# Kernel tuning notes

Measured on AMD Instinct MI355X. Metric: run time of the kernel, lower is better.

Reference implementation:

```python
import jax, jax.numpy as jnp
import numpy as np
import math

D_COV = 3      # covs = ['pi','juros','ipca']
WIDTH = 64     # largura default of RedeDrift/RedeDiff
T = 1024       # n_janela
I0 = 1
N_MC = 32768


def _linear_init(key, fan_in, fan_out):
    # torch nn.Linear default: U(-1/sqrt(fan_in), 1/sqrt(fan_in))
    bound = 1.0 / np.sqrt(fan_in)
    kw, kb = jax.random.split(key)
    W = jax.random.uniform(kw, (fan_in, fan_out), jnp.float32, -bound, bound)
    b = jax.random.uniform(kb, (fan_out,), jnp.float32, -bound, bound)
    return W, b


def setup_inputs() -> dict:
    key = jax.random.key(0)
    ks = jax.random.split(key, 12)
    d_in = 1 + D_COV + 1
    dW1, db1 = _linear_init(ks[0], d_in, WIDTH)
    dW2, db2 = _linear_init(ks[1], WIDTH, WIDTH)
    dW3, db3 = _linear_init(ks[2], WIDTH, 1)
    gW1, gb1 = _linear_init(ks[3], d_in, WIDTH)
    gW2, gb2 = _linear_init(ks[4], WIDTH, WIDTH)
    gW3, gb3 = _linear_init(ks[5], WIDTH, 1)
    X_seq = jax.random.normal(ks[6], (I0 + T, D_COV), jnp.float32)
    y_seq = jax.random.uniform(ks[7], (I0 + T,), jnp.float32)
    xi = jax.random.normal(ks[8], (T, N_MC), jnp.float32)  # randn_like noise, one draw per step
    a = jax.random.normal(ks[9], (D_COV,), jnp.float32) * 0.1
    return dict(
        X_seq=X_seq, y_seq=y_seq,
        kappa=jnp.float32(0.8), a=a,
        b0=jnp.float32(0.0), b1=jnp.float32(0.0), b2=jnp.float32(0.0),
        S=jnp.float32(12.0), log_sigma_obs=jnp.float32(-3.0),
        dW1=dW1, db1=db1, dW2=dW2, db2=db2, dW3=dW3, db3=db3,
        gW1=gW1, gb1=gb1, gW2=gW2, gb2=gb2, gW3=gW3, gb3=gb3,
        xi=xi, i0=I0, dt=1, n_janela=T, n_mc=N_MC,
    )


def reference(X_seq, y_seq, kappa, a, b0, b1, b2, S, log_sigma_obs,
              dW1, db1, dW2, db2, dW3, db3,
              gW1, gb1, gW2, gb2, gW3, gb3,
              xi, i0, dt, n_janela, n_mc):
    T_ = n_janela
    d_cov = X_seq.shape[1]
    t_idx = jnp.arange(i0, i0 + T_, dtype=jnp.float32)  # [T]
    Xw = X_seq[i0:i0 + T_]                               # [T, d_cov]
    y_obs = y_seq[i0:i0 + T_]                            # [T]
    # i0 > 0 branch: z0 = logit(clamp(y_{i0-1}))
    y0 = jnp.clip(y_seq[i0 - 1], 1e-4, 1.0 - 1e-4)
    z0 = jnp.log(y0 / (1.0 - y0))
    z_init = jnp.full((n_mc, 1), z0, dtype=jnp.float32)
    sqrt_dt = math.sqrt(dt)
    two_pi = 2.0 * math.pi

    def mlp(inp, W1, B1, W2, B2, W3, B3):
        h = jax.nn.silu(inp @ W1 + B1)
        h = jax.nn.silu(h @ W2 + B2)
        return h @ W3 + B3

    def step(z, per_step):
        xk, tk, xik = per_step  # [d_cov], scalar, [n_mc]
        x = jnp.broadcast_to(xk, (n_mc, d_cov))
        t = jnp.full((n_mc, 1), tk, dtype=jnp.float32)
        cat = jnp.concatenate([z, x, t], axis=-1)  # [n_mc, 1+d_cov+1]
        # mu_base
        mu = (x @ a + b0 + b1 * jnp.sin(two_pi * tk / S)
              + b2 * jnp.cos(two_pi * tk / S))[:, None]  # [n_mc, 1]
        f_res = mlp(cat, dW1, db1, dW2, db2, dW3, db3)
        g = jax.nn.softplus(mlp(cat, gW1, gb1, gW2, gb2, gW3, gb3)) + 1e-6
        drift = kappa * (mu - z) + f_res
        z_next = z + drift * dt + g * sqrt_dt * xik[:, None]
        return z_next, jax.nn.sigmoid(z_next)[:, 0]

    _, U = jax.lax.scan(step, z_init, (Xw, t_idx, xi))  # U: [T, n_mc]
    sigma_obs = jnp.exp(log_sigma_obs) + 1e-8
    nll = 0.5 * ((y_obs[:, None] - U) ** 2 / sigma_obs ** 2 + 2.0 * log_sigma_obs)
    return nll.mean()
```

## Files before the change

### kernel.cpp

```cpp
#include <hip/hip_runtime.h>
#include <math.h>

#define NMC    32768
#define TSTEPS 1024
#define PPB    32
#define NBLK   (NMC / PPB)
#define TWO_PI 6.28318530717958647692f

typedef short bf16x8 __attribute__((ext_vector_type(8)));
typedef float f32x4  __attribute__((ext_vector_type(4)));

#define MFMA_B16(A, B, C) (C) = __builtin_amdgcn_mfma_f32_16x16x32_bf16((A), (B), (C), 0, 0, 0)

__device__ __forceinline__ float fsilu(float x) { return __fdividef(x, 1.0f + __expf(-x)); }
__device__ __forceinline__ unsigned fbits(float x){ union{float f;unsigned u;}c; c.f=x; return c.u; }
__device__ __forceinline__ float bitsf(unsigned u){ union{float f;unsigned u;}c; c.u=u; return c.f; }
__device__ __forceinline__ bf16x8 mk8(unsigned a,unsigned b,unsigned c,unsigned d){
  union{unsigned u[4]; bf16x8 s;} z; z.u[0]=a; z.u[1]=b; z.u[2]=c; z.u[3]=d; return z.s;
}

__device__ __forceinline__ void split3(const float e[8], bf16x8 &H, bf16x8 &M, bf16x8 &L) {
  unsigned dH[4], dM[4], dL[4];
  #pragma unroll
  for (int v = 0; v < 4; ++v) {
    const float a0 = e[2*v], a1 = e[2*v+1];
    const unsigned uH0 = fbits(a0) & 0xFFFF0000u, uH1 = fbits(a1) & 0xFFFF0000u;
    const float r10 = a0 - bitsf(uH0), r11 = a1 - bitsf(uH1);
    const unsigned uM0 = fbits(r10) & 0xFFFF0000u, uM1 = fbits(r11) & 0xFFFF0000u;
    const float r20 = r10 - bitsf(uM0), r21 = r11 - bitsf(uM1);
    dH[v] = uH1 | (uH0 >> 16);
    dM[v] = uM1 | (uM0 >> 16);
    dL[v] = (fbits(r21) & 0xFFFF0000u) | (fbits(r20) >> 16);
  }
  H = mk8(dH[0],dH[1],dH[2],dH[3]);
  M = mk8(dM[0],dM[1],dM[2],dM[3]);
  L = mk8(dL[0],dL[1],dL[2],dL[3]);
}

__global__ __launch_bounds__(64) void init_out(float* __restrict__ out,
                                               const float* __restrict__ lso_p) {
  if (threadIdx.x == 0) *out = *lso_p;
}

__global__ __launch_bounds__(256) void sde_kernel(
    const float* __restrict__ X_seq, const float* __restrict__ y_seq,
    const float* __restrict__ kappa_p, const float* __restrict__ a_p,
    const float* __restrict__ b0_p, const float* __restrict__ b1_p,
    const float* __restrict__ b2_p, const float* __restrict__ S_p,
    const float* __restrict__ lso_p,
    const float* __restrict__ dW1, const float* __restrict__ db1,
    const float* __restrict__ dW2, const float* __restrict__ db2,
    const float* __restrict__ dW3, const float* __restrict__ db3,
    const float* __restrict__ gW1, const float* __restrict__ gb1,
    const float* __restrict__ gW2, const float* __restrict__ gb2,
    const float* __restrict__ gW3, const float* __restrict__ gb3,
    const float* __restrict__ xi,
    const int* __restrict__ i0_p, const int* __restrict__ dt_p,
    float* __restrict__ out)
{
  __shared__ __align__(16) float preLDS[2][64];
  __shared__ float part[2][PPB];

  const int tid    = threadIdx.x;
  const int l      = tid & 63;
  const int lane15 = l & 15;
  const int lg     = l >> 4;
  const int w      = __builtin_amdgcn_readfirstlane(tid >> 6);
  const int m      = w >> 1;
  const int pt     = w & 1;
  const int path_l = pt * 16 + lane15;
  const int gpath  = blockIdx.x * PPB + path_l;

  const float* W1 = m ? gW1 : dW1;
  const float* B1 = m ? gb1 : db1;
  const float* W2 = m ? gW2 : dW2;
  const float* B2 = m ? gb2 : db2;
  const float* W3 = m ? gW3 : dW3;

  const float kappa = *kappa_p;
  const float a0 = a_p[0], a1 = a_p[1], a2 = a_p[2];
  const float b0 = *b0_p, b1c = *b1_p, b2c = *b2_p, S = *S_p, lso = *lso_p;
  const int   i0 = *i0_p;
  const float dtf  = (float)(*dt_p);
  const float sqdt = sqrtf(dtf);
  const float db3v = db3[0], gb3v = gb3[0];

  const float b1v  = B1[l];
  const float w1r1 = W1[1*64 + l], w1r2 = W1[2*64 + l];
  const float w1r3 = W1[3*64 + l], w1r4 = W1[4*64 + l];

  float w1z[2][8];
  #pragma unroll
  for (int c = 0; c < 2; ++c)
    #pragma unroll
    for (int q = 0; q < 8; ++q)
      w1z[c][q] = W1[c*32 + lg*8 + q];

  float b2v[4], w3v[4];
  #pragma unroll
  for (int jt = 0; jt < 4; ++jt) {
    b2v[jt] = B2[jt*16 + lane15];
    w3v[jt] = W3[jt*16 + lane15];
  }

  bf16x8 bH[2][4], bM[2][4], bL[2][4];
  #pragma unroll
  for (int c = 0; c < 2; ++c)
    #pragma unroll
    for (int jt = 0; jt < 4; ++jt) {
      float e[8];
      #pragma unroll
      for (int q = 0; q < 8; ++q)
        e[q] = W2[(c*32 + lg*8 + q)*64 + jt*16 + lane15];
      split3(e, bH[c][jt], bM[c][jt], bL[c][jt]);
    }

  float y0 = y_seq[i0 - 1];
  y0 = fminf(fmaxf(y0, 1e-4f), 1.0f - 1e-4f);
  float z = logf(y0 / (1.0f - y0));
  float nacc = 0.0f;

  float x0 = X_seq[i0*3 + 0], x1 = X_seq[i0*3 + 1], x2 = X_seq[i0*3 + 2];
  float yk  = y_seq[i0];
  float xik = xi[gpath];

  #pragma unroll 1
  for (int t = 0; t < TSTEPS; ++t) {
    const float tk = (float)(i0 + t);

    if (pt == 0) {
      const float pv = fmaf(tk, w1r4, fmaf(x2, w1r3, fmaf(x1, w1r2, fmaf(x0, w1r1, b1v))));
      preLDS[m][l] = pv;
    }
    __syncthreads();

    const int tn = (t + 1 < TSTEPS) ? t + 1 : t;
    const float xn0 = X_seq[(i0+tn)*3 + 0];
    const float xn1 = X_seq[(i0+tn)*3 + 1];
    const float xn2 = X_seq[(i0+tn)*3 + 2];
    const float yn  = y_seq[i0 + tn];
    const float xin = xi[tn*NMC + gpath];

    bf16x8 aH[2], aM[2], aL[2];
    #pragma unroll
    for (int c = 0; c < 2; ++c) {
      const f32x4 p0 = *reinterpret_cast<const f32x4*>(&preLDS[m][c*32 + lg*8 + 0]);
      const f32x4 p1 = *reinterpret_cast<const f32x4*>(&preLDS[m][c*32 + lg*8 + 4]);
      float e[8];
      e[0] = fsilu(fmaf(z, w1z[c][0], p0[0]));
      e[1] = fsilu(fmaf(z, w1z[c][1], p0[1]));
      e[2] = fsilu(fmaf(z, w1z[c][2], p0[2]));
      e[3] = fsilu(fmaf(z, w1z[c][3], p0[3]));
      e[4] = fsilu(fmaf(z, w1z[c][4], p1[0]));
      e[5] = fsilu(fmaf(z, w1z[c][5], p1[1]));
      e[6] = fsilu(fmaf(z, w1z[c][6], p1[2]));
      e[7] = fsilu(fmaf(z, w1z[c][7], p1[3]));
      split3(e, aH[c], aM[c], aL[c]);
    }

    f32x4 acc[4];
    #pragma unroll
    for (int jt = 0; jt < 4; ++jt) {
      acc[jt][0] = b2v[jt]; acc[jt][1] = b2v[jt];
      acc[jt][2] = b2v[jt]; acc[jt][3] = b2v[jt];
    }
    #pragma unroll
    for (int c = 0; c < 2; ++c) {
      #pragma unroll
      for (int jt = 0; jt < 4; ++jt) {
        MFMA_B16(aH[c], bH[c][jt], acc[jt]);
        MFMA_B16(aH[c], bM[c][jt], acc[jt]);
        MFMA_B16(aM[c], bH[c][jt], acc[jt]);
        MFMA_B16(aH[c], bL[c][jt], acc[jt]);
        MFMA_B16(aL[c], bH[c][jt], acc[jt]);
        MFMA_B16(aM[c], bM[c][jt], acc[jt]);
      }
    }

    float s0 = 0.0f, s1 = 0.0f, s2 = 0.0f, s3 = 0.0f;
    #pragma unroll
    for (int jt = 0; jt < 4; ++jt) {
      s0 = fmaf(fsilu(acc[jt][0]), w3v[jt], s0);
      s1 = fmaf(fsilu(acc[jt][1]), w3v[jt], s1);
      s2 = fmaf(fsilu(acc[jt][2]), w3v[jt], s2);
      s3 = fmaf(fsilu(acc[jt][3]), w3v[jt], s3);
    }
    #pragma unroll
    for (int off = 1; off < 16; off <<= 1) {
      s0 += __shfl_xor(s0, off, 64);
      s1 += __shfl_xor(s1, off, 64);
      s2 += __shfl_xor(s2, off, 64);
      s3 += __shfl_xor(s3, off, 64);
    }
    const float sv = lane15 == 0 ? s0 : lane15 == 1 ? s1 : lane15 == 2 ? s2 : s3;
    if (lane15 < 4) part[m][pt*16 + lg*4 + lane15] = sv;
    __syncthreads();

    const float f  = part[0][path_l] + db3v;
    const float gp = part[1][path_l] + gb3v;
    const float ax = fabsf(gp);
    const float g  = fmaxf(gp, 0.0f) + __logf(1.0f + __expf(-ax)) + 1e-6f;

    const float ang = TWO_PI * tk / S;
    const float mu  = fmaf(x0, a0, fmaf(x1, a1, x2 * a2)) + b0
                      + b1c * __sinf(ang) + b2c * __cosf(ang);
    z = z + (kappa * (mu - z) + f) * dtf + g * sqdt * xik;

    if (m == 0 && lg == 0) {
      const float U = __fdividef(1.0f, 1.0f + __expf(-z));
      const float d = yk - U;
      nacc = fmaf(d, d, nacc);
    }

    x0 = xn0; x1 = xn1; x2 = xn2; yk = yn; xik = xin;
  }

  if (m == 0) {
    float v = nacc;
    #pragma unroll
    for (int off = 1; off < 64; off <<= 1) v += __shfl_xor(v, off, 64);
    if (l == 0) {
      const float sobs  = __expf(lso) + 1e-8f;
      const float scale = 0.5f / (sobs * sobs) / ((float)TSTEPS * (float)NMC);
      atomicAdd(out, v * scale);
    }
  }
}

extern "C" void kernel_launch(void* const* d_in, const int* in_sizes, int n_in,
                              void* d_out, int out_size, void* d_ws, size_t ws_size,
                              hipStream_t stream) {
  const float* X_seq = (const float*)d_in[0];
  const float* y_seq = (const float*)d_in[1];
  const float* kappa = (const float*)d_in[2];
  const float* a     = (const float*)d_in[3];
  const float* b0    = (const float*)d_in[4];
  const float* b1    = (const float*)d_in[5];
  const float* b2    = (const float*)d_in[6];
  const float* S     = (const float*)d_in[7];
  const float* lso   = (const float*)d_in[8];
  const float* dW1   = (const float*)d_in[9];
  const float* db1   = (const float*)d_in[10];
  const float* dW2   = (const float*)d_in[11];
  const float* db2   = (const float*)d_in[12];
  const float* dW3   = (const float*)d_in[13];
  const float* db3   = (const float*)d_in[14];
  const float* gW1   = (const float*)d_in[15];
  const float* gb1   = (const float*)d_in[16];
  const float* gW2   = (const float*)d_in[17];
  const float* gb2   = (const float*)d_in[18];
  const float* gW3   = (const float*)d_in[19];
  const float* gb3   = (const float*)d_in[20];
  const float* xi    = (const float*)d_in[21];
  const int*   i0    = (const int*)d_in[22];
  const int*   dt    = (const int*)d_in[23];
  float* out = (float*)d_out;

  hipLaunchKernelGGL(init_out, dim3(1), dim3(64), 0, stream, out, lso);
  hipLaunchKernelGGL(sde_kernel, dim3(NBLK), dim3(256), 0, stream,
                     X_seq, y_seq, kappa, a, b0, b1, b2, S, lso,
                     dW1, db1, dW2, db2, dW3, db3,
                     gW1, gb1, gW2, gb2, gW3, gb3,
                     xi, i0, dt, out);
}
```

Baseline: 6.733 ms.

## Make each wave evaluate both MLPs for its paths, removing per-step block barriers

Each wave now owns 16 paths and runs both the drift and diffusion MLPs itself, so the two per-step __syncthreads and the LDS exchange of partial sums go away. The time-dependent first-layer pre-activations are computed once by a new pre_kernel into workspace and read from global memory each step. The split bf16 W2 fragments move from registers into shared memory to make room for doubled per-wave work. In exchange each wave does twice the MFMA and activation work per step, reads W2 fragments from LDS every step, and launch bounds now request two blocks per CU.

```diff
diff --git a/kernel.cpp b/kernel.cpp
--- a/kernel.cpp
+++ b/kernel.cpp
@@ -3,7 +3,9 @@
 
 #define NMC    32768
 #define TSTEPS 1024
-#define PPB    32
+#define PPW    16
+#define WPB    4
+#define PPB    (PPW*WPB)
 #define NBLK   (NMC / PPB)
 #define TWO_PI 6.28318530717958647692f
 
@@ -42,40 +44,53 @@
   if (threadIdx.x == 0) *out = *lso_p;
 }
 
-__global__ __launch_bounds__(256) void sde_kernel(
+__global__ __launch_bounds__(256) void pre_kernel(
+    const float* __restrict__ X_seq,
+    const float* __restrict__ dW1, const float* __restrict__ db1,
+    const float* __restrict__ gW1, const float* __restrict__ gb1,
+    const int* __restrict__ i0_p, float* __restrict__ pre)
+{
+  const int g = blockIdx.x * 256 + threadIdx.x;
+  const int t = g >> 7;
+  const int m = (g >> 6) & 1;
+  const int k = g & 63;
+  const float* W1 = m ? gW1 : dW1;
+  const float* B1 = m ? gb1 : db1;
+  const int i0 = *i0_p;
+  const float tk = (float)(i0 + t);
+  const float x0 = X_seq[(i0+t)*3 + 0];
+  const float x1 = X_seq[(i0+t)*3 + 1];
+  const float x2 = X_seq[(i0+t)*3 + 2];
+  pre[g] = fmaf(tk, W1[4*64 + k],
+           fmaf(x2, W1[3*64 + k],
+           fmaf(x1, W1[2*64 + k],
+           fmaf(x0, W1[1*64 + k], B1[k]))));
+}
+
+__global__ __launch_bounds__(256, 2) void sde_kernel(
     const float* __restrict__ X_seq, const float* __restrict__ y_seq,
     const float* __restrict__ kappa_p, const float* __restrict__ a_p,
     const float* __restrict__ b0_p, const float* __restrict__ b1_p,
     const float* __restrict__ b2_p, const float* __restrict__ S_p,
     const float* __restrict__ lso_p,
-    const float* __restrict__ dW1, const float* __restrict__ db1,
+    const float* __restrict__ dW1,
     const float* __restrict__ dW2, const float* __restrict__ db2,
     const float* __restrict__ dW3, const float* __restrict__ db3,
-    const float* __restrict__ gW1, const float* __restrict__ gb1,
+    const float* __restrict__ gW1,
     const float* __restrict__ gW2, const float* __restrict__ gb2,
     const float* __restrict__ gW3, const float* __restrict__ gb3,
-    const float* __restrict__ xi,
+    const float* __restrict__ xi, const float* __restrict__ pre,
     const int* __restrict__ i0_p, const int* __restrict__ dt_p,
     float* __restrict__ out)
 {
-  __shared__ __align__(16) float preLDS[2][64];
-  __shared__ float part[2][PPB];
+  __shared__ bf16x8 Bf[2][3][2][4][64];
 
   const int tid    = threadIdx.x;
   const int l      = tid & 63;
   const int lane15 = l & 15;
   const int lg     = l >> 4;
   const int w      = __builtin_amdgcn_readfirstlane(tid >> 6);
-  const int m      = w >> 1;
-  const int pt     = w & 1;
-  const int path_l = pt * 16 + lane15;
-  const int gpath  = blockIdx.x * PPB + path_l;
-
-  const float* W1 = m ? gW1 : dW1;
-  const float* B1 = m ? gb1 : db1;
-  const float* W2 = m ? gW2 : dW2;
-  const float* B2 = m ? gb2 : db2;
-  const float* W3 = m ? gW3 : dW3;
+  const int gpath  = blockIdx.x * PPB + w * PPW + lane15;
 
   const float kappa = *kappa_p;
   const float a0 = a_p[0], a1 = a_p[1], a2 = a_p[2];
@@ -85,35 +100,45 @@
   const float sqdt = sqrtf(dtf);
   const float db3v = db3[0], gb3v = gb3[0];
 
-  const float b1v  = B1[l];
-  const float w1r1 = W1[1*64 + l], w1r2 = W1[2*64 + l];
-  const float w1r3 = W1[3*64 + l], w1r4 = W1[4*64 + l];
-
-  float w1z[2][8];
-  #pragma unroll
-  for (int c = 0; c < 2; ++c)
+  #pragma unroll
+  for (int gi = 0; gi < 4; ++gi) {
+    const int gidx = w * 4 + gi;
+    const int bm = gidx >> 3, bc = (gidx >> 2) & 1, bjt = gidx & 3;
+    const float* W2 = bm ? gW2 : dW2;
+    float e[8];
     #pragma unroll
     for (int q = 0; q < 8; ++q)
-      w1z[c][q] = W1[c*32 + lg*8 + q];
-
-  float b2v[4], w3v[4];
-  #pragma unroll
-  for (int jt = 0; jt < 4; ++jt) {
-    b2v[jt] = B2[jt*16 + lane15];
-    w3v[jt] = W3[jt*16 + lane15];
-  }
-
-  bf16x8 bH[2][4], bM[2][4], bL[2][4];
-  #pragma unroll
-  for (int c = 0; c < 2; ++c)
+      e[q] = W2[(bc*32 + lg*8 + q)*64 + bjt*16 + lane15];
+    bf16x8 H, M, L;
+    split3(e, H, M, L);
+    Bf[bm][0][bc][bjt][l] = H;
+    Bf[bm][1][bc][bjt][l] = M;
+    Bf[bm][2][bc][bjt][l] = L;
+  }
+
+  float w1z[2][2][8];
+  #pragma unroll
+  for (int mm = 0; mm < 2; ++mm) {
+    const float* W1 = mm ? gW1 : dW1;
+    #pragma unroll
+    for (int c = 0; c < 2; ++c)
+      #pragma unroll
+      for (int q = 0; q < 8; ++q)
+        w1z[mm][c][q] = W1[c*32 + lg*8 + q];
+  }
+  float b2v[2][4], w3v[2][4];
+  #pragma unroll
+  for (int mm = 0; mm < 2; ++mm) {
+    const float* B2 = mm ? gb2 : db2;
+    const float* W3 = mm ? gW3 : dW3;
     #pragma unroll
     for (int jt = 0; jt < 4; ++jt) {
-      float e[8];
-      #pragma unroll
-      for (int q = 0; q < 8; ++q)
-        e[q] = W2[(c*32 + lg*8 + q)*64 + jt*16 + lane15];
-      split3(e, bH[c][jt], bM[c][jt], bL[c][jt]);
+      b2v[mm][jt] = B2[jt*16 + lane15];
+      w3v[mm][jt] = W3[jt*16 + lane15];
     }
+  }
+
+  __syncthreads();
 
   float y0 = y_seq[i0 - 1];
   y0 = fminf(fmaxf(y0, 1e-4f), 1.0f - 1e-4f);
@@ -128,76 +153,86 @@
   for (int t = 0; t < TSTEPS; ++t) {
     const float tk = (float)(i0 + t);
 
-    if (pt == 0) {
-      const float pv = fmaf(tk, w1r4, fmaf(x2, w1r3, fmaf(x1, w1r2, fmaf(x0, w1r1, b1v))));
-      preLDS[m][l] = pv;
-    }
-    __syncthreads();
+    f32x4 pr[2][2][2];
+    const float* pb = pre + (size_t)t * 128;
+    #pragma unroll
+    for (int mm = 0; mm < 2; ++mm)
+      #pragma unroll
+      for (int c = 0; c < 2; ++c) {
+        const f32x4* pp = reinterpret_cast<const f32x4*>(pb + mm*64 + c*32 + lg*8);
+        pr[mm][c][0] = pp[0];
+        pr[mm][c][1] = pp[1];
+      }
 
     const int tn = (t + 1 < TSTEPS) ? t + 1 : t;
     const float xn0 = X_seq[(i0+tn)*3 + 0];
     const float xn1 = X_seq[(i0+tn)*3 + 1];
     const float xn2 = X_seq[(i0+tn)*3 + 2];
     const float yn  = y_seq[i0 + tn];
-    const float xin = xi[tn*NMC + gpath];
-
-    bf16x8 aH[2], aM[2], aL[2];
-    #pragma unroll
-    for (int c = 0; c < 2; ++c) {
-      const f32x4 p0 = *reinterpret_cast<const f32x4*>(&preLDS[m][c*32 + lg*8 + 0]);
-      const f32x4 p1 = *reinterpret_cast<const f32x4*>(&preLDS[m][c*32 + lg*8 + 4]);
-      float e[8];
-      e[0] = fsilu(fmaf(z, w1z[c][0], p0[0]));
-      e[1] = fsilu(fmaf(z, w1z[c][1], p0[1]));
-      e[2] = fsilu(fmaf(z, w1z[c][2], p0[2]));
-      e[3] = fsilu(fmaf(z, w1z[c][3], p0[3]));
-      e[4] = fsilu(fmaf(z, w1z[c][4], p1[0]));
-      e[5] = fsilu(fmaf(z, w1z[c][5], p1[1]));
-      e[6] = fsilu(fmaf(z, w1z[c][6], p1[2]));
-      e[7] = fsilu(fmaf(z, w1z[c][7], p1[3]));
-      split3(e, aH[c], aM[c], aL[c]);
+    const float xin = xi[(size_t)tn*NMC + gpath];
+
+    float fg[2];
+    #pragma unroll
+    for (int mm = 0; mm < 2; ++mm) {
+      bf16x8 aH[2], aM[2], aL[2];
+      #pragma unroll
+      for (int c = 0; c < 2; ++c) {
+        float e[8];
+        #pragma unroll
+        for (int q = 0; q < 4; ++q)
+          e[q] = fsilu(fmaf(z, w1z[mm][c][q], pr[mm][c][0][q]));
+        #pragma unroll
+        for (int q = 0; q < 4; ++q)
+          e[4+q] = fsilu(fmaf(z, w1z[mm][c][4+q], pr[mm][c][1][q]));
+        split3(e, aH[c], aM[c], aL[c]);
+      }
+
+      f32x4 acc[4];
+      #pragma unroll
+      for (int jt = 0; jt < 4; ++jt) {
+        acc[jt][0] = b2v[mm][jt]; acc[jt][1] = b2v[mm][jt];
+        acc[jt][2] = b2v[mm][jt]; acc[jt][3] = b2v[mm][jt];
+      }
+      #pragma unroll
+      for (int c = 0; c < 2; ++c) {
+        #pragma unroll
+        for (int jt = 0; jt < 4; ++jt) {
+          const bf16x8 bh = Bf[mm][0][c][jt][l];
+          const bf16x8 bm_ = Bf[mm][1][c][jt][l];
+          const bf16x8 bl = Bf[mm][2][c][jt][l];
+          MFMA_B16(aH[c], bh,  acc[jt]);
+          MFMA_B16(aH[c], bm_, acc[jt]);
+          MFMA_B16(aM[c], bh,  acc[jt]);
+          MFMA_B16(aH[c], bl,  acc[jt]);
+          MFMA_B16(aL[c], bh,  acc[jt]);
+          MFMA_B16(aM[c], bm_, acc[jt]);
+        }
+      }
+
+      float s0 = 0.0f, s1 = 0.0f, s2 = 0.0f, s3 = 0.0f;
+      #pragma unroll
+      for (int jt = 0; jt < 4; ++jt) {
+        s0 = fmaf(fsilu(acc[jt][0]), w3v[mm][jt], s0);
+        s1 = fmaf(fsilu(acc[jt][1]), w3v[mm][jt], s1);
+        s2 = fmaf(fsilu(acc[jt][2]), w3v[mm][jt], s2);
+        s3 = fmaf(fsilu(acc[jt][3]), w3v[mm][jt], s3);
+      }
+      const float a01 = (lane15 & 1) ? s1 : s0;
+      const float b01 = (lane15 & 1) ? s0 : s1;
+      float u  = a01 + __shfl_xor(b01, 1, 64);
+      const float a23 = (lane15 & 1) ? s3 : s2;
+      const float b23 = (lane15 & 1) ? s2 : s3;
+      float u2 = a23 + __shfl_xor(b23, 1, 64);
+      const float aw = (lane15 & 2) ? u2 : u;
+      const float bw = (lane15 & 2) ? u  : u2;
+      float wv = aw + __shfl_xor(bw, 2, 64);
+      wv += __shfl_xor(wv, 4, 64);
+      wv += __shfl_xor(wv, 8, 64);
+      fg[mm] = __shfl(wv, (lane15 >> 2) * 16 + (lane15 & 3), 64);
     }
 
-    f32x4 acc[4];
-    #pragma unroll
-    for (int jt = 0; jt < 4; ++jt) {
-      acc[jt][0] = b2v[jt]; acc[jt][1] = b2v[jt];
-      acc[jt][2] = b2v[jt]; acc[jt][3] = b2v[jt];
-    }
-    #pragma unroll
-    for (int c = 0; c < 2; ++c) {
-      #pragma unroll
-      for (int jt = 0; jt < 4; ++jt) {
-        MFMA_B16(aH[c], bH[c][jt], acc[jt]);
-        MFMA_B16(aH[c], bM[c][jt], acc[jt]);
-        MFMA_B16(aM[c], bH[c][jt], acc[jt]);
-        MFMA_B16(aH[c], bL[c][jt], acc[jt]);
-        MFMA_B16(aL[c], bH[c][jt], acc[jt]);
-        MFMA_B16(aM[c], bM[c][jt], acc[jt]);
-      }
-    }
-
-    float s0 = 0.0f, s1 = 0.0f, s2 = 0.0f, s3 = 0.0f;
-    #pragma unroll
-    for (int jt = 0; jt < 4; ++jt) {
-      s0 = fmaf(fsilu(acc[jt][0]), w3v[jt], s0);
-      s1 = fmaf(fsilu(acc[jt][1]), w3v[jt], s1);
-      s2 = fmaf(fsilu(acc[jt][2]), w3v[jt], s2);
-      s3 = fmaf(fsilu(acc[jt][3]), w3v[jt], s3);
-    }
-    #pragma unroll
-    for (int off = 1; off < 16; off <<= 1) {
-      s0 += __shfl_xor(s0, off, 64);
-      s1 += __shfl_xor(s1, off, 64);
-      s2 += __shfl_xor(s2, off, 64);
-      s3 += __shfl_xor(s3, off, 64);
-    }
-    const float sv = lane15 == 0 ? s0 : lane15 == 1 ? s1 : lane15 == 2 ? s2 : s3;
-    if (lane15 < 4) part[m][pt*16 + lg*4 + lane15] = sv;
-    __syncthreads();
-
-    const float f  = part[0][path_l] + db3v;
-    const float gp = part[1][path_l] + gb3v;
+    const float f  = fg[0] + db3v;
+    const float gp = fg[1] + gb3v;
     const float ax = fabsf(gp);
     const float g  = fmaxf(gp, 0.0f) + __logf(1.0f + __expf(-ax)) + 1e-6f;
 
@@ -206,7 +241,7 @@
                       + b1c * __sinf(ang) + b2c * __cosf(ang);
     z = z + (kappa * (mu - z) + f) * dtf + g * sqdt * xik;
 
-    if (m == 0 && lg == 0) {
+    if (lg == 0) {
       const float U = __fdividef(1.0f, 1.0f + __expf(-z));
       const float d = yk - U;
       nacc = fmaf(d, d, nacc);
@@ -215,15 +250,13 @@
     x0 = xn0; x1 = xn1; x2 = xn2; yk = yn; xik = xin;
   }
 
-  if (m == 0) {
-    float v = nacc;
-    #pragma unroll
-    for (int off = 1; off < 64; off <<= 1) v += __shfl_xor(v, off, 64);
-    if (l == 0) {
-      const float sobs  = __expf(lso) + 1e-8f;
-      const float scale = 0.5f / (sobs * sobs) / ((float)TSTEPS * (float)NMC);
-      atomicAdd(out, v * scale);
-    }
+  float v = nacc;
+  #pragma unroll
+  for (int off = 1; off < 64; off <<= 1) v += __shfl_xor(v, off, 64);
+  if (l == 0) {
+    const float sobs  = __expf(lso) + 1e-8f;
+    const float scale = 0.5f / (sobs * sobs) / ((float)TSTEPS * (float)NMC);
+    atomicAdd(out, v * scale);
   }
 }
 
@@ -255,11 +288,14 @@
   const int*   i0    = (const int*)d_in[22];
   const int*   dt    = (const int*)d_in[23];
   float* out = (float*)d_out;
+  float* pre = (float*)d_ws;
 
   hipLaunchKernelGGL(init_out, dim3(1), dim3(64), 0, stream, out, lso);
+  hipLaunchKernelGGL(pre_kernel, dim3(512), dim3(256), 0, stream,
+                     X_seq, dW1, db1, gW1, gb1, i0, pre);
   hipLaunchKernelGGL(sde_kernel, dim3(NBLK), dim3(256), 0, stream,
                      X_seq, y_seq, kappa, a, b0, b1, b2, S, lso,
-                     dW1, db1, dW2, db2, dW3, db3,
-                     gW1, gb1, gW2, gb2, gW3, gb3,
-                     xi, i0, dt, out);
-}
+                     dW1, dW2, db2, dW3, db3,
+                     gW1, gW2, gb2, gW3, gb3,
+                     xi, pre, i0, dt, out);
+}
```

Result: slower. 11.43 ms (+69.8%).
